# Kernel tuning notes

Measured on AMD Instinct MI355X. Metric: run time of the kernel, lower is better.

The kernel has to match this reference:

```python
import jax, jax.numpy as jnp
import numpy as np

B, S, H = 256, 1, 2048
Q_SIZE = 4096        # num_heads * head_dim = 32 * 128
QKV = 4 * H          # expected_linear_qkv = 8192
K_SZ = 4             # conv kernel size
C = 32               # ssm channels
WSCALE = 0.02


def setup_inputs() -> dict:
    key = jax.random.key(0)
    ks = jax.random.split(key, 13)
    return {
        "hidden_states": jax.random.normal(ks[0], (B, S, H), jnp.float32),
        "W_qkv": jax.random.normal(ks[1], (QKV, H), jnp.float32) * WSCALE,
        "b_qkv": jax.random.normal(ks[2], (QKV,), jnp.float32) * WSCALE,
        "W_gate": jax.random.normal(ks[3], (2 * H, H), jnp.float32) * WSCALE,
        "W_alpha": jax.random.normal(ks[4], (C, H), jnp.float32) * WSCALE,
        "W_beta": jax.random.normal(ks[5], (C, H), jnp.float32) * WSCALE,
        "W_out": jax.random.normal(ks[6], (H, 2 * H), jnp.float32) * WSCALE,
        "ssm_state_a": jax.random.normal(ks[7], (C,), jnp.float32),
        "ssm_dt_bias": jax.random.normal(ks[8], (C,), jnp.float32),
        "ssm_norm_weight": jnp.ones((128,), jnp.float32),
        "conv_kernel": jax.random.normal(ks[9], (QKV, K_SZ), jnp.float32) * WSCALE,
        "ssm_state": jax.random.normal(ks[10], (B, C), jnp.float32),
        "conv_state": jax.random.normal(ks[11], (B, K_SZ, QKV), jnp.float32),
    }


def reference(hidden_states, W_qkv, b_qkv, W_gate, W_alpha, W_beta, W_out,
              ssm_state_a, ssm_dt_bias, ssm_norm_weight, conv_kernel,
              ssm_state, conv_state):
    bsz = hidden_states.shape[0]
    # qkv projection (decode: only last token matters downstream)
    qkv = jnp.einsum('bsh,dh->bsd', hidden_states, W_qkv) + b_qkv  # [B,S,4H]
    mixed_qkv = qkv[:, -1, :].astype(jnp.float32)                  # [B,4H]
    hidden_last = hidden_states[:, -1, :]                          # [B,H]

    # roll conv state and append current token, then causal conv1d step
    cs = jnp.concatenate([conv_state[:, 1:, :], mixed_qkv[:, None, :]], axis=1)  # [B,K,4H]
    conv_out = jnp.einsum('bkd,dk->bd', cs, conv_kernel)           # [B,4H]

    target_size = conv_out.shape[-1] - Q_SIZE                      # 2H = 4096
    k_size = target_size // 2                                      # 2048
    core_base = conv_out[:, Q_SIZE:]                               # [B,2H]
    k_proj = core_base[:, :k_size]
    v_proj = core_base[:, k_size:]

    # alpha/beta gating of the SSM state
    a = hidden_last @ W_alpha.T                                    # [B,C]
    b = hidden_last @ W_beta.T                                     # [B,C]
    g = -jnp.exp(ssm_state_a)[None, :] * jax.nn.softplus(a + ssm_dt_bias[None, :])
    beta = jax.nn.sigmoid(b)

    group_width = k_size // C                                      # 64
    v_group = v_proj[:, :group_width * C].reshape(bsz, C, group_width).mean(-1)
    k_group = k_proj[:, :group_width * C].reshape(bsz, C, group_width).mean(-1)

    new_state = jnp.exp(g) * ssm_state + beta * v_group            # [B,C]
    state_signal = new_state * jax.nn.sigmoid(k_group)             # [B,C]

    repeat_factor = target_size // C                               # 128
    expanded = jnp.repeat(state_signal, repeat_factor, axis=-1)[:, :target_size]

    core = core_base + expanded
    core = core * jax.lax.rsqrt(jnp.mean(core * core, axis=-1, keepdims=True) + 1e-6)
    gate = jax.nn.sigmoid(hidden_last @ W_gate.T).astype(jnp.float32)
    core = core * gate * jnp.mean(ssm_norm_weight)
    core = core.astype(hidden_states.dtype)

    out = (core @ W_out.T)[:, None, :]                             # [B,1,H]
    return out
```

## Files before the change

### kernel.cpp

```cpp
#include <hip/hip_runtime.h>
#include <hip/hip_bf16.h>
#include <stdint.h>

#define BSZ 256
#define NQ 4096
#define N1 8320
#define K1 2048
#define N3 2048
#define K3 4096

typedef __attribute__((ext_vector_type(8))) short bf16x8;
typedef __attribute__((ext_vector_type(4))) float f32x4;

__device__ __forceinline__ unsigned short f2bf(float f) {
  union { float f; unsigned u; } v; v.f = f;
  unsigned r = v.u + 0x7fffu + ((v.u >> 16) & 1u);
  return (unsigned short)(r >> 16);
}

__device__ __forceinline__ bf16x8 pack8(float4 a, float4 b) {
  union { bf16x8 v; unsigned short u[8]; } o;
  o.u[0] = f2bf(a.x); o.u[1] = f2bf(a.y); o.u[2] = f2bf(a.z); o.u[3] = f2bf(a.w);
  o.u[4] = f2bf(b.x); o.u[5] = f2bf(b.y); o.u[6] = f2bf(b.z); o.u[7] = f2bf(b.w);
  return o.v;
}

__device__ __forceinline__ void gload_lds16(const void* g, void* lds_uniform) {
  __builtin_amdgcn_global_load_lds(
      (const __attribute__((address_space(1))) unsigned int*)g,
      (__attribute__((address_space(3))) unsigned int*)lds_uniform, 16, 0, 0);
}

__global__ __launch_bounds__(256) void cvt_kernel(const float* __restrict__ x,
                                                  unsigned short* __restrict__ y) {
  int i = (blockIdx.x * 256 + threadIdx.x) * 8;
  float4 a = *(const float4*)(x + i);
  float4 b = *(const float4*)(x + i + 4);
  ushort4 o0 = { f2bf(a.x), f2bf(a.y), f2bf(a.z), f2bf(a.w) };
  ushort4 o1 = { f2bf(b.x), f2bf(b.y), f2bf(b.z), f2bf(b.w) };
  *(ushort4*)(y + i) = o0;
  *(ushort4*)(y + i + 4) = o1;
}


__global__ __launch_bounds__(256, 4) void gemm1_kernel(
    const unsigned short* __restrict__ A16,
    const float* __restrict__ Wqkv, const float* __restrict__ Wgate,
    const float* __restrict__ Walpha, const float* __restrict__ Wbeta,
    float* __restrict__ P) {
  __shared__ __align__(16) unsigned short sA[128 * 64];
  __shared__ __align__(16) float sB[32 * 64];
  const int tid = threadIdx.x, lane = tid & 63, wv = tid >> 6;
  const int wr = wv >> 1, wc = wv & 1, l15 = lane & 15;
  const int rt = blockIdx.x * 128;
  const int n0 = blockIdx.y * 32;
  const int kb = blockIdx.z * 1024;

  const char* aS[4]; char* aD[4];
#pragma unroll
  for (int t = 0; t < 4; t++) {
    int s = wv * 4 + t;
    int m = 8 * s + (lane >> 3);
    int c = (lane & 7) ^ ((lane >> 3) & 7);
    aS[t] = (const char*)(A16 + (size_t)(rt + m) * K1 + kb) + c * 16;
    aD[t] = (char*)sA + s * 1024;
  }
  const char* bS[2]; char* bD[2];
#pragma unroll
  for (int t = 0; t < 2; t++) {
    int s = wv * 2 + t;
    int n = 4 * s + (lane >> 4);
    int c = (lane & 15) ^ (n & 15);
    int ng = n0 + n;
    const float* base;
    if (ng < 4096)       base = Wqkv  + (size_t)(4096 + ng) * K1;
    else if (ng < 8192)  base = Wgate + (size_t)(ng - 4096) * K1;
    else if (ng < 8224)  base = Walpha + (size_t)(ng - 8192) * K1;
    else if (ng < 8256)  base = Wbeta + (size_t)(ng - 8224) * K1;
    else                 base = Walpha;
    bS[t] = (const char*)(base + kb) + c * 16;
    bD[t] = (char*)sB + s * 1024;
  }

  f32x4 acc[4];
#pragma unroll
  for (int i = 0; i < 4; i++) { f32x4 z = {0.f, 0.f, 0.f, 0.f}; acc[i] = z; }

  for (int it = 0; it < 16; it++) {
    __syncthreads();
#pragma unroll
    for (int t = 0; t < 4; t++) gload_lds16(aS[t] + it * 128, aD[t]);
#pragma unroll
    for (int t = 0; t < 2; t++) gload_lds16(bS[t] + it * 256, bD[t]);
    __syncthreads();
#pragma unroll
    for (int ks2 = 0; ks2 < 2; ks2++) {
      int nr = wc * 16 + l15;
      int c0 = ks2 * 8 + (lane >> 4) * 2;
      float4 b0 = *(const float4*)((const char*)sB + nr * 256 + ((c0 ^ (nr & 15)) * 16));
      float4 b1 = *(const float4*)((const char*)sB + nr * 256 + (((c0 + 1) ^ (nr & 15)) * 16));
      bf16x8 bF = pack8(b0, b1);
#pragma unroll
      for (int i = 0; i < 4; i++) {
        int m = wr * 64 + i * 16 + l15;
        int cA = ks2 * 4 + (lane >> 4);
        bf16x8 aF = *(const bf16x8*)((const char*)sA + m * 128 + ((cA ^ (m & 7)) * 16));
        acc[i] = __builtin_amdgcn_mfma_f32_16x16x32_bf16(aF, bF, acc[i], 0, 0, 0);
      }
    }
  }

  float* Pz = P + (size_t)blockIdx.z * ((size_t)BSZ * N1);
#pragma unroll
  for (int i = 0; i < 4; i++) {
    int row = rt + wr * 64 + i * 16 + (lane >> 4) * 4;
    int col = n0 + wc * 16 + l15;
#pragma unroll
    for (int r = 0; r < 4; r++)
      Pz[(size_t)(row + r) * N1 + col] = acc[i][r];
  }
}

__global__ __launch_bounds__(512) void fuse_kernel(
    const float* __restrict__ P,
    const float* __restrict__ bqkv,
    const float* __restrict__ ck,
    const float* __restrict__ cstate,
    const float* __restrict__ ssa,
    const float* __restrict__ dtb,
    const float* __restrict__ nw,
    const float* __restrict__ sstate,
    unsigned short* __restrict__ C16) {
  __shared__ __align__(16) float cb[4096];
  __shared__ float gsum[64];
  __shared__ float ssl[32];
  __shared__ float red[16];
  const int b = blockIdx.x, tid = threadIdx.x;
  const int lane = tid & 63, wv = tid >> 6;
  const float* P0 = P + (size_t)b * N1;
  const float* P1 = P + (size_t)(BSZ + b) * N1;

  if (wv == 0) {
    float m = nw[lane] + nw[lane + 64];
#pragma unroll
    for (int off = 32; off; off >>= 1) m += __shfl_down(m, off, 64);
    if (lane == 0) red[8] = m * (1.f / 128.f);
  }

#pragma unroll
  for (int it = 0; it < 2; it++) {
    int j = (it * 512 + tid) * 4;
    float4 q0 = *(const float4*)(P0 + j);
    float4 q1 = *(const float4*)(P1 + j);
    float4 bq = *(const float4*)(bqkv + NQ + j);
    float mqx = q0.x + q1.x + bq.x, mqy = q0.y + q1.y + bq.y;
    float mqz = q0.z + q1.z + bq.z, mqw = q0.w + q1.w + bq.w;
    const float* csb = cstate + (size_t)b * 4 * 8192 + NQ + j;
    float4 c1 = *(const float4*)(csb + 8192);
    float4 c2 = *(const float4*)(csb + 16384);
    float4 c3 = *(const float4*)(csb + 24576);
    float4 k0v = *(const float4*)(ck + (size_t)(NQ + j) * 4);
    float4 k1v = *(const float4*)(ck + (size_t)(NQ + j + 1) * 4);
    float4 k2v = *(const float4*)(ck + (size_t)(NQ + j + 2) * 4);
    float4 k3v = *(const float4*)(ck + (size_t)(NQ + j + 3) * 4);
    float4 cbv;
    cbv.x = c1.x * k0v.x + c2.x * k0v.y + c3.x * k0v.z + mqx * k0v.w;
    cbv.y = c1.y * k1v.x + c2.y * k1v.y + c3.y * k1v.z + mqy * k1v.w;
    cbv.z = c1.z * k2v.x + c2.z * k2v.y + c3.z * k2v.z + mqz * k2v.w;
    cbv.w = c1.w * k3v.x + c2.w * k3v.y + c3.w * k3v.z + mqw * k3v.w;
    *(float4*)(cb + j) = cbv;
    float s = cbv.x + cbv.y + cbv.z + cbv.w;
    s += __shfl_xor(s, 1, 64); s += __shfl_xor(s, 2, 64);
    s += __shfl_xor(s, 4, 64); s += __shfl_xor(s, 8, 64);
    if ((lane & 15) == 0) gsum[(it * 512 + tid) >> 4] = s;
  }
  __syncthreads();

  if (tid < 32) {
    float a  = P0[8192 + tid] + P1[8192 + tid];
    float bc = P0[8224 + tid] + P1[8224 + tid];
    float kg = gsum[tid] * (1.f / 64.f);
    float vg = gsum[32 + tid] * (1.f / 64.f);
    float x = a + dtb[tid];
    float sp = fmaxf(x, 0.f) + log1pf(expf(-fabsf(x)));
    float g = -expf(ssa[tid]) * sp;
    float beta = 1.f / (1.f + expf(-bc));
    float ns = expf(g) * sstate[b * 32 + tid] + beta * vg;
    ssl[tid] = ns / (1.f + expf(-kg));
  }
  __syncthreads();

  float sq = 0.f;
  float4 c1r[2];
#pragma unroll
  for (int it = 0; it < 2; it++) {
    int j = (it * 512 + tid) * 4;
    float4 v = *(const float4*)(cb + j);
    float sv = ssl[j >> 7];
    v.x += sv; v.y += sv; v.z += sv; v.w += sv;
    c1r[it] = v;
    sq += v.x * v.x + v.y * v.y + v.z * v.z + v.w * v.w;
  }
#pragma unroll
  for (int off = 32; off; off >>= 1) sq += __shfl_down(sq, off, 64);
  if (lane == 0) red[wv] = sq;
  __syncthreads();
  if (tid == 0) {
    float t = red[0] + red[1] + red[2] + red[3] + red[4] + red[5] + red[6] + red[7];
    red[9] = rsqrtf(t * (1.f / 4096.f) + 1e-6f);
  }
  __syncthreads();
  float rms = red[9], mwv = red[8];

#pragma unroll
  for (int it = 0; it < 2; it++) {
    int j = (it * 512 + tid) * 4;
    float4 g0x = *(const float4*)(P0 + NQ + j);
    float4 g1x = *(const float4*)(P1 + NQ + j);
    float4 v = c1r[it];
    float ox = v.x * rms * mwv / (1.f + expf(-(g0x.x + g1x.x)));
    float oy = v.y * rms * mwv / (1.f + expf(-(g0x.y + g1x.y)));
    float oz = v.z * rms * mwv / (1.f + expf(-(g0x.z + g1x.z)));
    float ow = v.w * rms * mwv / (1.f + expf(-(g0x.w + g1x.w)));
    ushort4 u = { f2bf(ox), f2bf(oy), f2bf(oz), f2bf(ow) };
    *(ushort4*)(C16 + (size_t)b * 4096 + j) = u;
  }
}

__global__ __launch_bounds__(256, 4) void gemm3_kernel(
    const unsigned short* __restrict__ A16,
    const float* __restrict__ Wout,
    float* __restrict__ OP) {
  __shared__ __align__(16) unsigned short sA[128 * 64];
  __shared__ __align__(16) float sB[32 * 64];
  const int tid = threadIdx.x, lane = tid & 63, wv = tid >> 6;
  const int wr = wv >> 1, wc = wv & 1, l15 = lane & 15;
  const int rt = blockIdx.x * 128;
  const int n0 = blockIdx.y * 32;
  const int kb = blockIdx.z * 512;

  const char* aS[4]; char* aD[4];
#pragma unroll
  for (int t = 0; t < 4; t++) {
    int s = wv * 4 + t;
    int m = 8 * s + (lane >> 3);
    int c = (lane & 7) ^ ((lane >> 3) & 7);
    aS[t] = (const char*)(A16 + (size_t)(rt + m) * K3 + kb) + c * 16;
    aD[t] = (char*)sA + s * 1024;
  }
  const char* bS[2]; char* bD[2];
#pragma unroll
  for (int t = 0; t < 2; t++) {
    int s = wv * 2 + t;
    int n = 4 * s + (lane >> 4);
    int c = (lane & 15) ^ (n & 15);
    bS[t] = (const char*)(Wout + (size_t)(n0 + n) * K3 + kb) + c * 16;
    bD[t] = (char*)sB + s * 1024;
  }

  f32x4 acc[4];
#pragma unroll
  for (int i = 0; i < 4; i++) { f32x4 z = {0.f, 0.f, 0.f, 0.f}; acc[i] = z; }

  for (int it = 0; it < 8; it++) {
    __syncthreads();
#pragma unroll
    for (int t = 0; t < 4; t++) gload_lds16(aS[t] + it * 128, aD[t]);
#pragma unroll
    for (int t = 0; t < 2; t++) gload_lds16(bS[t] + it * 256, bD[t]);
    __syncthreads();
#pragma unroll
    for (int ks2 = 0; ks2 < 2; ks2++) {
      int nr = wc * 16 + l15;
      int c0 = ks2 * 8 + (lane >> 4) * 2;
      float4 b0 = *(const float4*)((const char*)sB + nr * 256 + ((c0 ^ (nr & 15)) * 16));
      float4 b1 = *(const float4*)((const char*)sB + nr * 256 + (((c0 + 1) ^ (nr & 15)) * 16));
      bf16x8 bF = pack8(b0, b1);
#pragma unroll
      for (int i = 0; i < 4; i++) {
        int m = wr * 64 + i * 16 + l15;
        int cA = ks2 * 4 + (lane >> 4);
        bf16x8 aF = *(const bf16x8*)((const char*)sA + m * 128 + ((cA ^ (m & 7)) * 16));
        acc[i] = __builtin_amdgcn_mfma_f32_16x16x32_bf16(aF, bF, acc[i], 0, 0, 0);
      }
    }
  }

  float* Oz = OP + (size_t)blockIdx.z * ((size_t)BSZ * N3);
#pragma unroll
  for (int i = 0; i < 4; i++) {
    int row = rt + wr * 64 + i * 16 + (lane >> 4) * 4;
    int col = n0 + wc * 16 + l15;
#pragma unroll
    for (int r = 0; r < 4; r++)
      Oz[(size_t)(row + r) * N3 + col] = acc[i][r];
  }
}

__global__ __launch_bounds__(256) void reduce_kernel(const float* __restrict__ OP,
                                                     float* __restrict__ out) {
  int i = (blockIdx.x * 256 + threadIdx.x) * 4;
  float4 s = *(const float4*)(OP + i);
#pragma unroll
  for (int z = 1; z < 8; z++) {
    float4 v = *(const float4*)(OP + (size_t)z * BSZ * N3 + i);
    s.x += v.x; s.y += v.y; s.z += v.z; s.w += v.w;
  }
  *(float4*)(out + i) = s;
}

extern "C" void kernel_launch(void* const* d_in, const int* in_sizes, int n_in,
                              void* d_out, int out_size, void* d_ws, size_t ws_size,
                              hipStream_t stream) {
  const float* hidden = (const float*)d_in[0];
  const float* Wqkv   = (const float*)d_in[1];
  const float* bqkv   = (const float*)d_in[2];
  const float* Wgate  = (const float*)d_in[3];
  const float* Walpha = (const float*)d_in[4];
  const float* Wbeta  = (const float*)d_in[5];
  const float* Wout   = (const float*)d_in[6];
  const float* ssa    = (const float*)d_in[7];
  const float* dtb    = (const float*)d_in[8];
  const float* nw     = (const float*)d_in[9];
  const float* ck     = (const float*)d_in[10];
  const float* sstate = (const float*)d_in[11];
  const float* cstate = (const float*)d_in[12];
  float* out = (float*)d_out;

  char* ws = (char*)d_ws;
  unsigned short* A16 = (unsigned short*)ws;
  float* P   = (float*)(ws + (1 << 20));
  unsigned short* C16 = (unsigned short*)(ws + (1 << 20) + 17039360);
  float* OP  = (float*)(ws + (1 << 20) + 17039360 + (2 << 20));

  cvt_kernel<<<256, 256, 0, stream>>>(hidden, A16);
  gemm1_kernel<<<dim3(2, 260, 2), 256, 0, stream>>>(A16, Wqkv, Wgate, Walpha, Wbeta, P);
  fuse_kernel<<<256, 512, 0, stream>>>(P, bqkv, ck, cstate, ssa, dtb, nw, sstate, C16);
  gemm3_kernel<<<dim3(2, 64, 8), 256, 0, stream>>>(C16, Wout, OP);
  reduce_kernel<<<512, 256, 0, stream>>>(OP, out);
}
```

Baseline: 233.4 us.

## Register-prefetch double-buffered LDS pipeline in GEMMs; convert B to bf16 before LDS

```diff
diff --git a/kernel.cpp b/kernel.cpp
--- a/kernel.cpp
+++ b/kernel.cpp
@@ -25,10 +25,9 @@
   return o.v;
 }
 
-__device__ __forceinline__ void gload_lds16(const void* g, void* lds_uniform) {
-  __builtin_amdgcn_global_load_lds(
-      (const __attribute__((address_space(1))) unsigned int*)g,
-      (__attribute__((address_space(3))) unsigned int*)lds_uniform, 16, 0, 0);
+__device__ __forceinline__ void barrier_lgkm_only() {
+  asm volatile("s_waitcnt lgkmcnt(0)" ::: "memory");
+  asm volatile("s_barrier" ::: "memory");
 }
 
 __global__ __launch_bounds__(256) void cvt_kernel(const float* __restrict__ x,
@@ -48,65 +47,70 @@
     const float* __restrict__ Wqkv, const float* __restrict__ Wgate,
     const float* __restrict__ Walpha, const float* __restrict__ Wbeta,
     float* __restrict__ P) {
-  __shared__ __align__(16) unsigned short sA[128 * 64];
-  __shared__ __align__(16) float sB[32 * 64];
+  __shared__ __align__(16) char sA[2][8192];
+  __shared__ __align__(16) char sB[2][2112];
   const int tid = threadIdx.x, lane = tid & 63, wv = tid >> 6;
-  const int wr = wv >> 1, wc = wv & 1, l15 = lane & 15;
+  const int wr = wv >> 1, wc = wv & 1, l15 = lane & 15, q = lane >> 4;
   const int rt = blockIdx.x * 128;
   const int n0 = blockIdx.y * 32;
   const int kb = blockIdx.z * 1024;
 
-  const char* aS[4]; char* aD[4];
-#pragma unroll
-  for (int t = 0; t < 4; t++) {
-    int s = wv * 4 + t;
-    int m = 8 * s + (lane >> 3);
-    int c = (lane & 7) ^ ((lane >> 3) & 7);
-    aS[t] = (const char*)(A16 + (size_t)(rt + m) * K1 + kb) + c * 16;
-    aD[t] = (char*)sA + s * 1024;
-  }
-  const char* bS[2]; char* bD[2];
-#pragma unroll
-  for (int t = 0; t < 2; t++) {
-    int s = wv * 2 + t;
-    int n = 4 * s + (lane >> 4);
-    int c = (lane & 15) ^ (n & 15);
-    int ng = n0 + n;
+  const int am = tid >> 1, ah = tid & 1;
+  const char* pA = (const char*)(A16 + (size_t)(rt + am) * K1 + kb) + ah * 32;
+  const int axor = (am >> 3) & 3;
+  const int aoff0 = (((2 * ah) ^ axor) * 2048) + am * 16;
+  const int aoff1 = (((2 * ah + 1) ^ axor) * 2048) + am * 16;
+
+  const bool doB = (tid < 128);
+  const int bn = tid >> 2, bp = tid & 3;
+  const float* pB = Walpha;
+  if (doB) {
+    int ng = n0 + bn;
     const float* base;
     if (ng < 4096)       base = Wqkv  + (size_t)(4096 + ng) * K1;
     else if (ng < 8192)  base = Wgate + (size_t)(ng - 4096) * K1;
     else if (ng < 8224)  base = Walpha + (size_t)(ng - 8192) * K1;
     else if (ng < 8256)  base = Wbeta + (size_t)(ng - 8224) * K1;
     else                 base = Walpha;
-    bS[t] = (const char*)(base + kb) + c * 16;
-    bD[t] = (char*)sB + s * 1024;
+    pB = base + kb + bp * 8;
+  }
+  const int boff = ((bp ^ (bn & 3)) * 528) + bn * 16;
+
+  const int nr = wc * 16 + l15;
+  const int cboff = ((q ^ (nr & 3)) * 528) + nr * 16;
+  int caoff[4];
+#pragma unroll
+  for (int i = 0; i < 4; i++) {
+    int m = wr * 64 + i * 16 + l15;
+    caoff[i] = ((q ^ ((m >> 3) & 3)) * 2048) + m * 16;
   }
 
   f32x4 acc[4];
 #pragma unroll
   for (int i = 0; i < 4; i++) { f32x4 z = {0.f, 0.f, 0.f, 0.f}; acc[i] = z; }
 
-  for (int it = 0; it < 16; it++) {
-    __syncthreads();
-#pragma unroll
-    for (int t = 0; t < 4; t++) gload_lds16(aS[t] + it * 128, aD[t]);
-#pragma unroll
-    for (int t = 0; t < 2; t++) gload_lds16(bS[t] + it * 256, bD[t]);
-    __syncthreads();
-#pragma unroll
-    for (int ks2 = 0; ks2 < 2; ks2++) {
-      int nr = wc * 16 + l15;
-      int c0 = ks2 * 8 + (lane >> 4) * 2;
-      float4 b0 = *(const float4*)((const char*)sB + nr * 256 + ((c0 ^ (nr & 15)) * 16));
-      float4 b1 = *(const float4*)((const char*)sB + nr * 256 + (((c0 + 1) ^ (nr & 15)) * 16));
-      bf16x8 bF = pack8(b0, b1);
-#pragma unroll
-      for (int i = 0; i < 4; i++) {
-        int m = wr * 64 + i * 16 + l15;
-        int cA = ks2 * 4 + (lane >> 4);
-        bf16x8 aF = *(const bf16x8*)((const char*)sA + m * 128 + ((cA ^ (m & 7)) * 16));
-        acc[i] = __builtin_amdgcn_mfma_f32_16x16x32_bf16(aF, bF, acc[i], 0, 0, 0);
-      }
+  uint4 a0 = *(const uint4*)pA;
+  uint4 a1 = *(const uint4*)(pA + 16);
+  float4 b0, b1;
+  if (doB) { b0 = *(const float4*)pB; b1 = *(const float4*)(pB + 4); }
+
+  for (int it = 0; it < 32; it++) {
+    char* sAb = sA[it & 1]; char* sBb = sB[it & 1];
+    *(uint4*)(sAb + aoff0) = a0;
+    *(uint4*)(sAb + aoff1) = a1;
+    if (doB) *(bf16x8*)(sBb + boff) = pack8(b0, b1);
+    if (it + 1 < 32) {
+      pA += 64;
+      a0 = *(const uint4*)pA;
+      a1 = *(const uint4*)(pA + 16);
+      if (doB) { pB += 32; b0 = *(const float4*)pB; b1 = *(const float4*)(pB + 4); }
+    }
+    barrier_lgkm_only();
+    bf16x8 bF = *(const bf16x8*)(sBb + cboff);
+#pragma unroll
+    for (int i = 0; i < 4; i++) {
+      bf16x8 aF = *(const bf16x8*)(sAb + caoff[i]);
+      acc[i] = __builtin_amdgcn_mfma_f32_16x16x32_bf16(aF, bF, acc[i], 0, 0, 0);
     }
   }
 
@@ -121,7 +125,7 @@
   }
 }
 
-__global__ __launch_bounds__(512) void fuse_kernel(
+__global__ __launch_bounds__(1024) void fuse_kernel(
     const float* __restrict__ P,
     const float* __restrict__ bqkv,
     const float* __restrict__ ck,
@@ -131,48 +135,48 @@
     const float* __restrict__ nw,
     const float* __restrict__ sstate,
     unsigned short* __restrict__ C16) {
-  __shared__ __align__(16) float cb[4096];
   __shared__ float gsum[64];
   __shared__ float ssl[32];
-  __shared__ float red[16];
+  __shared__ float red[20];
   const int b = blockIdx.x, tid = threadIdx.x;
   const int lane = tid & 63, wv = tid >> 6;
   const float* P0 = P + (size_t)b * N1;
   const float* P1 = P + (size_t)(BSZ + b) * N1;
+  const int j = tid * 4;
+
+  float4 g0x = *(const float4*)(P0 + NQ + j);
+  float4 g1x = *(const float4*)(P1 + NQ + j);
 
   if (wv == 0) {
     float m = nw[lane] + nw[lane + 64];
 #pragma unroll
     for (int off = 32; off; off >>= 1) m += __shfl_down(m, off, 64);
-    if (lane == 0) red[8] = m * (1.f / 128.f);
-  }
-
-#pragma unroll
-  for (int it = 0; it < 2; it++) {
-    int j = (it * 512 + tid) * 4;
-    float4 q0 = *(const float4*)(P0 + j);
-    float4 q1 = *(const float4*)(P1 + j);
-    float4 bq = *(const float4*)(bqkv + NQ + j);
-    float mqx = q0.x + q1.x + bq.x, mqy = q0.y + q1.y + bq.y;
-    float mqz = q0.z + q1.z + bq.z, mqw = q0.w + q1.w + bq.w;
-    const float* csb = cstate + (size_t)b * 4 * 8192 + NQ + j;
-    float4 c1 = *(const float4*)(csb + 8192);
-    float4 c2 = *(const float4*)(csb + 16384);
-    float4 c3 = *(const float4*)(csb + 24576);
-    float4 k0v = *(const float4*)(ck + (size_t)(NQ + j) * 4);
-    float4 k1v = *(const float4*)(ck + (size_t)(NQ + j + 1) * 4);
-    float4 k2v = *(const float4*)(ck + (size_t)(NQ + j + 2) * 4);
-    float4 k3v = *(const float4*)(ck + (size_t)(NQ + j + 3) * 4);
-    float4 cbv;
-    cbv.x = c1.x * k0v.x + c2.x * k0v.y + c3.x * k0v.z + mqx * k0v.w;
-    cbv.y = c1.y * k1v.x + c2.y * k1v.y + c3.y * k1v.z + mqy * k1v.w;
-    cbv.z = c1.z * k2v.x + c2.z * k2v.y + c3.z * k2v.z + mqz * k2v.w;
-    cbv.w = c1.w * k3v.x + c2.w * k3v.y + c3.w * k3v.z + mqw * k3v.w;
-    *(float4*)(cb + j) = cbv;
+    if (lane == 0) red[16] = m * (1.f / 128.f);
+  }
+
+  float4 q0 = *(const float4*)(P0 + j);
+  float4 q1 = *(const float4*)(P1 + j);
+  float4 bq = *(const float4*)(bqkv + NQ + j);
+  float mqx = q0.x + q1.x + bq.x, mqy = q0.y + q1.y + bq.y;
+  float mqz = q0.z + q1.z + bq.z, mqw = q0.w + q1.w + bq.w;
+  const float* csb = cstate + (size_t)b * 4 * 8192 + NQ + j;
+  float4 c1 = *(const float4*)(csb + 8192);
+  float4 c2 = *(const float4*)(csb + 16384);
+  float4 c3 = *(const float4*)(csb + 24576);
+  float4 k0v = *(const float4*)(ck + (size_t)(NQ + j) * 4);
+  float4 k1v = *(const float4*)(ck + (size_t)(NQ + j + 1) * 4);
+  float4 k2v = *(const float4*)(ck + (size_t)(NQ + j + 2) * 4);
+  float4 k3v = *(const float4*)(ck + (size_t)(NQ + j + 3) * 4);
+  float4 cbv;
+  cbv.x = c1.x * k0v.x + c2.x * k0v.y + c3.x * k0v.z + mqx * k0v.w;
+  cbv.y = c1.y * k1v.x + c2.y * k1v.y + c3.y * k1v.z + mqy * k1v.w;
+  cbv.z = c1.z * k2v.x + c2.z * k2v.y + c3.z * k2v.z + mqz * k2v.w;
+  cbv.w = c1.w * k3v.x + c2.w * k3v.y + c3.w * k3v.z + mqw * k3v.w;
+  {
     float s = cbv.x + cbv.y + cbv.z + cbv.w;
     s += __shfl_xor(s, 1, 64); s += __shfl_xor(s, 2, 64);
     s += __shfl_xor(s, 4, 64); s += __shfl_xor(s, 8, 64);
-    if ((lane & 15) == 0) gsum[(it * 512 + tid) >> 4] = s;
+    if ((lane & 15) == 0) gsum[tid >> 4] = s;
   }
   __syncthreads();
 
@@ -190,99 +194,89 @@
   }
   __syncthreads();
 
-  float sq = 0.f;
-  float4 c1r[2];
-#pragma unroll
-  for (int it = 0; it < 2; it++) {
-    int j = (it * 512 + tid) * 4;
-    float4 v = *(const float4*)(cb + j);
-    float sv = ssl[j >> 7];
-    v.x += sv; v.y += sv; v.z += sv; v.w += sv;
-    c1r[it] = v;
-    sq += v.x * v.x + v.y * v.y + v.z * v.z + v.w * v.w;
-  }
+  float sv = ssl[j >> 7];
+  float4 v = cbv;
+  v.x += sv; v.y += sv; v.z += sv; v.w += sv;
+  float sq = v.x * v.x + v.y * v.y + v.z * v.z + v.w * v.w;
 #pragma unroll
   for (int off = 32; off; off >>= 1) sq += __shfl_down(sq, off, 64);
   if (lane == 0) red[wv] = sq;
   __syncthreads();
   if (tid == 0) {
-    float t = red[0] + red[1] + red[2] + red[3] + red[4] + red[5] + red[6] + red[7];
-    red[9] = rsqrtf(t * (1.f / 4096.f) + 1e-6f);
+    float t = 0.f;
+#pragma unroll
+    for (int w = 0; w < 16; w++) t += red[w];
+    red[17] = rsqrtf(t * (1.f / 4096.f) + 1e-6f);
   }
   __syncthreads();
-  float rms = red[9], mwv = red[8];
-
-#pragma unroll
-  for (int it = 0; it < 2; it++) {
-    int j = (it * 512 + tid) * 4;
-    float4 g0x = *(const float4*)(P0 + NQ + j);
-    float4 g1x = *(const float4*)(P1 + NQ + j);
-    float4 v = c1r[it];
-    float ox = v.x * rms * mwv / (1.f + expf(-(g0x.x + g1x.x)));
-    float oy = v.y * rms * mwv / (1.f + expf(-(g0x.y + g1x.y)));
-    float oz = v.z * rms * mwv / (1.f + expf(-(g0x.z + g1x.z)));
-    float ow = v.w * rms * mwv / (1.f + expf(-(g0x.w + g1x.w)));
-    ushort4 u = { f2bf(ox), f2bf(oy), f2bf(oz), f2bf(ow) };
-    *(ushort4*)(C16 + (size_t)b * 4096 + j) = u;
-  }
+  float rms = red[17], mwv = red[16];
+
+  float ox = v.x * rms * mwv / (1.f + expf(-(g0x.x + g1x.x)));
+  float oy = v.y * rms * mwv / (1.f + expf(-(g0x.y + g1x.y)));
+  float oz = v.z * rms * mwv / (1.f + expf(-(g0x.z + g1x.z)));
+  float ow = v.w * rms * mwv / (1.f + expf(-(g0x.w + g1x.w)));
+  ushort4 u = { f2bf(ox), f2bf(oy), f2bf(oz), f2bf(ow) };
+  *(ushort4*)(C16 + (size_t)b * 4096 + j) = u;
 }
 
 __global__ __launch_bounds__(256, 4) void gemm3_kernel(
     const unsigned short* __restrict__ A16,
     const float* __restrict__ Wout,
     float* __restrict__ OP) {
-  __shared__ __align__(16) unsigned short sA[128 * 64];
-  __shared__ __align__(16) float sB[32 * 64];
+  __shared__ __align__(16) char sA[2][8192];
+  __shared__ __align__(16) char sB[2][2112];
   const int tid = threadIdx.x, lane = tid & 63, wv = tid >> 6;
-  const int wr = wv >> 1, wc = wv & 1, l15 = lane & 15;
+  const int wr = wv >> 1, wc = wv & 1, l15 = lane & 15, q = lane >> 4;
   const int rt = blockIdx.x * 128;
   const int n0 = blockIdx.y * 32;
   const int kb = blockIdx.z * 512;
 
-  const char* aS[4]; char* aD[4];
-#pragma unroll
-  for (int t = 0; t < 4; t++) {
-    int s = wv * 4 + t;
-    int m = 8 * s + (lane >> 3);
-    int c = (lane & 7) ^ ((lane >> 3) & 7);
-    aS[t] = (const char*)(A16 + (size_t)(rt + m) * K3 + kb) + c * 16;
-    aD[t] = (char*)sA + s * 1024;
-  }
-  const char* bS[2]; char* bD[2];
-#pragma unroll
-  for (int t = 0; t < 2; t++) {
-    int s = wv * 2 + t;
-    int n = 4 * s + (lane >> 4);
-    int c = (lane & 15) ^ (n & 15);
-    bS[t] = (const char*)(Wout + (size_t)(n0 + n) * K3 + kb) + c * 16;
-    bD[t] = (char*)sB + s * 1024;
+  const int am = tid >> 1, ah = tid & 1;
+  const char* pA = (const char*)(A16 + (size_t)(rt + am) * K3 + kb) + ah * 32;
+  const int axor = (am >> 3) & 3;
+  const int aoff0 = (((2 * ah) ^ axor) * 2048) + am * 16;
+  const int aoff1 = (((2 * ah + 1) ^ axor) * 2048) + am * 16;
+
+  const bool doB = (tid < 128);
+  const int bn = tid >> 2, bp = tid & 3;
+  const float* pB = Wout + (size_t)(n0 + bn) * K3 + kb + bp * 8;
+  const int boff = ((bp ^ (bn & 3)) * 528) + bn * 16;
+
+  const int nr = wc * 16 + l15;
+  const int cboff = ((q ^ (nr & 3)) * 528) + nr * 16;
+  int caoff[4];
+#pragma unroll
+  for (int i = 0; i < 4; i++) {
+    int m = wr * 64 + i * 16 + l15;
+    caoff[i] = ((q ^ ((m >> 3) & 3)) * 2048) + m * 16;
   }
 
   f32x4 acc[4];
 #pragma unroll
   for (int i = 0; i < 4; i++) { f32x4 z = {0.f, 0.f, 0.f, 0.f}; acc[i] = z; }
 
-  for (int it = 0; it < 8; it++) {
-    __syncthreads();
-#pragma unroll
-    for (int t = 0; t < 4; t++) gload_lds16(aS[t] + it * 128, aD[t]);
-#pragma unroll
-    for (int t = 0; t < 2; t++) gload_lds16(bS[t] + it * 256, bD[t]);
-    __syncthreads();
-#pragma unroll
-    for (int ks2 = 0; ks2 < 2; ks2++) {
-      int nr = wc * 16 + l15;
-      int c0 = ks2 * 8 + (lane >> 4) * 2;
-      float4 b0 = *(const float4*)((const char*)sB + nr * 256 + ((c0 ^ (nr & 15)) * 16));
-      float4 b1 = *(const float4*)((const char*)sB + nr * 256 + (((c0 + 1) ^ (nr & 15)) * 16));
-      bf16x8 bF = pack8(b0, b1);
-#pragma unroll
-      for (int i = 0; i < 4; i++) {
-        int m = wr * 64 + i * 16 + l15;
-        int cA = ks2 * 4 + (lane >> 4);
-        bf16x8 aF = *(const bf16x8*)((const char*)sA + m * 128 + ((cA ^ (m & 7)) * 16));
-        acc[i] = __builtin_amdgcn_mfma_f32_16x16x32_bf16(aF, bF, acc[i], 0, 0, 0);
-      }
+  uint4 a0 = *(const uint4*)pA;
+  uint4 a1 = *(const uint4*)(pA + 16);
+  float4 b0, b1;
+  if (doB) { b0 = *(const float4*)pB; b1 = *(const float4*)(pB + 4); }
+
+  for (int it = 0; it < 16; it++) {
+    char* sAb = sA[it & 1]; char* sBb = sB[it & 1];
+    *(uint4*)(sAb + aoff0) = a0;
+    *(uint4*)(sAb + aoff1) = a1;
+    if (doB) *(bf16x8*)(sBb + boff) = pack8(b0, b1);
+    if (it + 1 < 16) {
+      pA += 64;
+      a0 = *(const uint4*)pA;
+      a1 = *(const uint4*)(pA + 16);
+      if (doB) { pB += 32; b0 = *(const float4*)pB; b1 = *(const float4*)(pB + 4); }
+    }
+    barrier_lgkm_only();
+    bf16x8 bF = *(const bf16x8*)(sBb + cboff);
+#pragma unroll
+    for (int i = 0; i < 4; i++) {
+      bf16x8 aF = *(const bf16x8*)(sAb + caoff[i]);
+      acc[i] = __builtin_amdgcn_mfma_f32_16x16x32_bf16(aF, bF, acc[i], 0, 0, 0);
     }
   }
 
@@ -335,7 +329,7 @@
 
   cvt_kernel<<<256, 256, 0, stream>>>(hidden, A16);
   gemm1_kernel<<<dim3(2, 260, 2), 256, 0, stream>>>(A16, Wqkv, Wgate, Walpha, Wbeta, P);
-  fuse_kernel<<<256, 512, 0, stream>>>(P, bqkv, ck, cstate, ssa, dtb, nw, sstate, C16);
+  fuse_kernel<<<256, 1024, 0, stream>>>(P, bqkv, ck, cstate, ssa, dtb, nw, sstate, C16);
   gemm3_kernel<<<dim3(2, 64, 8), 256, 0, stream>>>(C16, Wout, OP);
   reduce_kernel<<<512, 256, 0, stream>>>(OP, out);
 }
```

New measurement: 253.0 us. 1.08x slower.
